# Performance work log

Hardware: AMD Instinct MI355X
Metric: run time of the kernel (lower is better)

## Reference

```python
import jax, jax.numpy as jnp
import numpy as np

NUM_HEADS = 16
SIGMA_DATA = 1.0


def setup_inputs() -> dict:
    key = jax.random.key(0)
    ks = jax.random.split(key, 6)
    B, N, C = 4, 2048, 1024
    x = jax.random.normal(ks[0], (B, N, C), dtype=jnp.float32)
    t = jax.random.uniform(ks[1], (B,), dtype=jnp.float32)
    # Linear layers stored as (in, out) so y = x @ W + b
    Wqkv = jax.random.normal(ks[2], (C, 3 * C), dtype=jnp.float32) * (C ** -0.5)
    bqkv = jax.random.normal(ks[3], (3 * C,), dtype=jnp.float32) * 0.02
    Wproj = jax.random.normal(ks[4], (C, C), dtype=jnp.float32) * (C ** -0.5)
    bproj = jax.random.normal(ks[5], (C,), dtype=jnp.float32) * 0.02
    return {"x": x, "t": t, "Wqkv": Wqkv, "bqkv": bqkv, "Wproj": Wproj, "bproj": bproj}


def reference(x, t, Wqkv, bqkv, Wproj, bproj):
    B, N, C = x.shape
    H = NUM_HEADS
    Dh = C // H
    scale = Dh ** -0.5

    qkv = (x @ Wqkv + bqkv).reshape(B, N, 3, H, Dh)
    qkv = jnp.transpose(qkv, (2, 0, 3, 1, 4))
    q, k, v = qkv[0], qkv[1], qkv[2]

    # softmax attention
    scores = jnp.einsum("bhmd,bhnd->bhmn", q, k) * scale
    attn = jax.nn.softmax(scores, axis=-1)
    o = jnp.einsum("bhmn,bhnd->bhmd", attn, v)          # [B, H, N, Dh]
    o = jnp.transpose(o, (0, 2, 1, 3)).reshape(B, N, C)  # [B, N, C]

    # rCM skip coefficients; kernel launch collapses per-batch coeffs to their mean (scalar)
    sd2 = SIGMA_DATA ** 2
    c_skip = (sd2 / (t * t + sd2)).mean()
    c_out = (SIGMA_DATA * t / jnp.sqrt(sd2 + t * t)).mean()

    out = c_skip * x + c_out * o  # fused epilogue
    return out @ Wproj + bproj
```

## Files before the change

### kernel.cpp

```cpp
#include <hip/hip_runtime.h>


typedef unsigned short ushort_t;
typedef __bf16 bf16x8 __attribute__((ext_vector_type(8)));
typedef float f32x4 __attribute__((ext_vector_type(4)));

#define GAS __attribute__((address_space(1)))
#define LAS __attribute__((address_space(3)))

static __device__ __forceinline__ ushort_t f2bf(float f) {
  union { float f; unsigned int u; } v; v.f = f;
  unsigned int r = v.u + 0x7fffu + ((v.u >> 16) & 1u);
  return (ushort_t)(r >> 16);
}

static __device__ __forceinline__ void async16(const void* g, void* l) {
  __builtin_amdgcn_global_load_lds((const GAS unsigned int*)g,
                                   (LAS unsigned int*)l, 16, 0, 0);
}

__global__ __launch_bounds__(256) void prep_kernel(
    const float* __restrict__ x, ushort_t* __restrict__ Xbf,
    const float* __restrict__ Wqkv, ushort_t* __restrict__ WqkvT,
    const float* __restrict__ Wproj, ushort_t* __restrict__ WprojT) {
  __shared__ float tile[32][33];
  const int bid = (int)blockIdx.x, tid = threadIdx.x;
  if (bid < 8192) {
    int i = (bid * 256 + tid) * 4;
    float4 v = *(const float4*)(x + i);
    ushort4 o = make_ushort4(f2bf(v.x), f2bf(v.y), f2bf(v.z), f2bf(v.w));
    *(ushort4*)(Xbf + i) = o;
    return;
  }
  const float* in;
  ushort_t* out;
  int R, C, bx, by;
  if (bid < 11264) {
    int q = bid - 8192;
    by = q / 96; bx = q - by * 96;
    in = Wqkv; out = WqkvT; R = 1024; C = 3072;
  } else {
    int p = bid - 11264;
    bx = p & 31; by = p >> 5;
    in = Wproj; out = WprojT; R = 1024; C = 1024;
  }
  int bc = bx * 32, br = by * 32;
  int tx = tid & 31, ty = tid >> 5;
#pragma unroll
  for (int i = 0; i < 32; i += 8)
    tile[ty + i][tx] = in[(size_t)(br + ty + i) * C + bc + tx];
  __syncthreads();
#pragma unroll
  for (int i = 0; i < 32; i += 8)
    out[(size_t)(bc + ty + i) * R + br + tx] = f2bf(tile[tx][ty + i]);
}

static __device__ __forceinline__ void gemm128_core(
    const ushort_t* __restrict__ A, const ushort_t* __restrict__ Bt, int K,
    int m0, int n0, ushort_t* As, ushort_t* Bs, f32x4 acc[4][4]) {
  const int tid = threadIdx.x;
  const int wave = tid >> 6, lane = tid & 63;
  const int wm = (wave >> 1) * 64, wn = (wave & 1) * 64;
  const int lr = lane & 15, quad = lane >> 4;
  const int ch = ((quad + (lr >> 1)) & 3) * 8;
  for (int kb = 0; kb < K; kb += 32) {
#pragma unroll
    for (int i = 0; i < 2; ++i) {
      int c = (i * 4 + wave) * 64 + lane;
      int row = c >> 2;
      int cg = (((c & 3) - ((c >> 3) & 3)) & 3) * 8;
      async16(A + (size_t)(m0 + row) * K + kb + cg, As + (i * 4 + wave) * 512);
      async16(Bt + (size_t)(n0 + row) * K + kb + cg, Bs + (i * 4 + wave) * 512);
    }
    __syncthreads();
    bf16x8 af[4], bfr[4];
#pragma unroll
    for (int i = 0; i < 4; ++i) {
      af[i]  = *(const bf16x8*)(As + (wm + i * 16 + lr) * 32 + ch);
      bfr[i] = *(const bf16x8*)(Bs + (wn + i * 16 + lr) * 32 + ch);
    }
#pragma unroll
    for (int i = 0; i < 4; ++i)
#pragma unroll
      for (int j = 0; j < 4; ++j)
        acc[i][j] = __builtin_amdgcn_mfma_f32_16x16x32_bf16(af[i], bfr[j], acc[i][j], 0, 0, 0);
    __syncthreads();
  }
}

__global__ __launch_bounds__(256) void gemm_qkv_kernel(
    const ushort_t* __restrict__ Xbf, const ushort_t* __restrict__ Wt,
    const float* __restrict__ bqkv, ushort_t* __restrict__ Qb,
    ushort_t* __restrict__ Kb, ushort_t* __restrict__ Vb) {
  __shared__ __align__(16) ushort_t As[128 * 32];
  __shared__ __align__(16) ushort_t Bs[128 * 32];
  const int m0 = (blockIdx.x & 63) << 7;
  const int n0 = (blockIdx.x >> 6) << 7;
  f32x4 acc[4][4];
#pragma unroll
  for (int i = 0; i < 4; ++i)
#pragma unroll
    for (int j = 0; j < 4; ++j) acc[i][j] = f32x4{0.f, 0.f, 0.f, 0.f};
  gemm128_core(Xbf, Wt, 1024, m0, n0, As, Bs, acc);

  const int tid = threadIdx.x, wave = tid >> 6, lane = tid & 63;
  const int wm = (wave >> 1) * 64, wn = (wave & 1) * 64;
  const int col = lane & 15, quad = lane >> 4;
  const int b = m0 >> 11;
  const float C1 = 0.18033688011112042f;
#pragma unroll
  for (int j = 0; j < 4; ++j) {
    int jc = n0 + wn + j * 16 + col;
    float bj = bqkv[jc];
    int which = jc >> 10, rem = jc & 1023;
    int hh = rem >> 6, d = rem & 63;
    if (which == 2) {
      size_t vb2 = ((size_t)(b * 16 + hh) * 64 + d) * 2048;
#pragma unroll
      for (int i = 0; i < 4; ++i) {
        int nbase = (m0 + wm + i * 16 + quad * 4) & 2047;
        int npos = (nbase & ~31) | (((nbase >> 2) & 3) << 3) | (((nbase >> 4) & 1) << 2);
        ushort4 pk = make_ushort4(f2bf(acc[i][j][0] + bj), f2bf(acc[i][j][1] + bj),
                                  f2bf(acc[i][j][2] + bj), f2bf(acc[i][j][3] + bj));
        *(ushort4*)(Vb + vb2 + npos) = pk;
      }
    } else {
      ushort_t* dst = which == 0 ? Qb : Kb;
      float sc = which == 0 ? C1 : 1.0f;
      size_t base = ((size_t)(b * 16 + hh) * 2048) * 64 + d;
#pragma unroll
      for (int i = 0; i < 4; ++i)
#pragma unroll
        for (int r = 0; r < 4; ++r) {
          int nseq = (m0 + wm + i * 16 + quad * 4 + r) & 2047;
          dst[base + (size_t)nseq * 64] = f2bf((acc[i][j][r] + bj) * sc);
        }
    }
  }
}

__global__ __launch_bounds__(256) void gemm_out_kernel(
    const ushort_t* __restrict__ Hbf, const ushort_t* __restrict__ Wt,
    const float* __restrict__ bproj, float* __restrict__ out) {
  __shared__ __align__(16) ushort_t As[128 * 32];
  __shared__ __align__(16) ushort_t Bs[128 * 32];
  const int m0 = (blockIdx.x & 63) << 7;
  const int n0 = (blockIdx.x >> 6) << 7;
  f32x4 acc[4][4];
#pragma unroll
  for (int i = 0; i < 4; ++i)
#pragma unroll
    for (int j = 0; j < 4; ++j) acc[i][j] = f32x4{0.f, 0.f, 0.f, 0.f};
  gemm128_core(Hbf, Wt, 1024, m0, n0, As, Bs, acc);

  const int tid = threadIdx.x, wave = tid >> 6, lane = tid & 63;
  const int wm = (wave >> 1) * 64, wn = (wave & 1) * 64;
  const int col = lane & 15, quad = lane >> 4;
#pragma unroll
  for (int j = 0; j < 4; ++j) {
    int jc = n0 + wn + j * 16 + col;
    float bj = bproj[jc];
#pragma unroll
    for (int i = 0; i < 4; ++i)
#pragma unroll
      for (int r = 0; r < 4; ++r) {
        int m = m0 + wm + i * 16 + quad * 4 + r;
        out[(size_t)m * 1024 + jc] = acc[i][j][r] + bj;
      }
  }
}

__global__ __launch_bounds__(256, 4) void attn_kernel(
    const ushort_t* __restrict__ Qb, const ushort_t* __restrict__ Kb,
    const ushort_t* __restrict__ Vb, const float* __restrict__ x,
    const float* __restrict__ t, ushort_t* __restrict__ Hbf) {
  __shared__ __align__(16) ushort_t Ks[2][64 * 64];
  __shared__ __align__(16) ushort_t Vs[2][64 * 64];

  const int tid = threadIdx.x, w = tid >> 6, lane = tid & 63;
  const int m = lane & 15, q = lane >> 4;
  const int bid = (int)blockIdx.x;
  const int wg = (bid & 7) * 128 + (bid >> 3);
  const int bh = wg >> 4, rowbase = ((wg & 15) << 7) + w * 32;

  const ushort_t* Qg = Qb + ((size_t)bh * 2048 + rowbase) * 64;
  const ushort_t* Kg = Kb + (size_t)bh * 2048 * 64;
  const ushort_t* Vg = Vb + (size_t)bh * 64 * 2048;

  bf16x8 qf[2][2];
#pragma unroll
  for (int qt = 0; qt < 2; ++qt) {
    qf[qt][0] = *(const bf16x8*)(Qg + (qt * 16 + m) * 64 + q * 8);
    qf[qt][1] = *(const bf16x8*)(Qg + (qt * 16 + m) * 64 + 32 + q * 8);
  }

  auto stage = [&](int kt, int buf) {
#pragma unroll
    for (int i = 0; i < 2; ++i) {
      int f = i * 256 + tid;
      int r = f >> 3, g = (f & 7) ^ (r & 7);
      async16(Kg + (size_t)(kt * 64 + r) * 64 + g * 8,
              Ks[buf] + (size_t)(i * 256 + w * 64) * 8);
    }
#pragma unroll
    for (int i = 0; i < 2; ++i) {
      int f = i * 256 + tid;
      int d = f >> 3, g = (f & 7) ^ (d & 7);
      async16(Vg + (size_t)d * 2048 + kt * 64 + g * 8,
              Vs[buf] + (size_t)(i * 256 + w * 64) * 8);
    }
  };
  stage(0, 0);

  f32x4 oacc[2][4], lacc[2];
#pragma unroll
  for (int qt = 0; qt < 2; ++qt) {
    lacc[qt] = f32x4{0.f, 0.f, 0.f, 0.f};
#pragma unroll
    for (int dt = 0; dt < 4; ++dt) oacc[qt][dt] = f32x4{0.f, 0.f, 0.f, 0.f};
  }

  const float C2 = -23.083120654223414f;
  const f32x4 c2v = {C2, C2, C2, C2};
  const int mk = m & 7;
  union { bf16x8 v; unsigned int u[4]; } onesu;
#pragma unroll
  for (int h = 0; h < 4; ++h) onesu.u[h] = 0x3F803F80u;
  const bf16x8 ones = onesu.v;

#pragma unroll 2
  for (int kt = 0; kt < 32; ++kt) {
    const int cur = kt & 1;
    __syncthreads();
    if (kt < 31) stage(kt + 1, cur ^ 1);
    const ushort_t* K0 = Ks[cur];
    const ushort_t* V0 = Vs[cur];

#pragma unroll
    for (int p = 0; p < 2; ++p) {
      f32x4 st[2][2];
#pragma unroll
      for (int sh = 0; sh < 2; ++sh) {
        int s = p * 2 + sh;
        bf16x8 kf0 = *(const bf16x8*)(K0 + (s * 16 + m) * 64 + (q ^ mk) * 8);
        bf16x8 kf1 = *(const bf16x8*)(K0 + (s * 16 + m) * 64 + ((q + 4) ^ mk) * 8);
#pragma unroll
        for (int qt = 0; qt < 2; ++qt) {
          f32x4 a = __builtin_amdgcn_mfma_f32_16x16x32_bf16(kf0, qf[qt][0], c2v, 0, 0, 0);
          st[sh][qt] = __builtin_amdgcn_mfma_f32_16x16x32_bf16(kf1, qf[qt][1], a, 0, 0, 0);
        }
      }
      bf16x8 pf[2];
#pragma unroll
      for (int qt = 0; qt < 2; ++qt) {
        float pv[8];
#pragma unroll
        for (int sh = 0; sh < 2; ++sh)
#pragma unroll
          for (int rr = 0; rr < 4; ++rr)
            pv[sh * 4 + rr] = __builtin_amdgcn_exp2f(st[sh][qt][rr]);
        union { bf16x8 v; unsigned int u[4]; } pk;
#pragma unroll
        for (int h = 0; h < 4; ++h)
          pk.u[h] = __builtin_amdgcn_perm(__float_as_uint(pv[2 * h + 1]),
                                          __float_as_uint(pv[2 * h]), 0x07060302);
        pf[qt] = pk.v;
      }
#pragma unroll
      for (int dt = 0; dt < 4; ++dt) {
        bf16x8 vf = *(const bf16x8*)(V0 + (dt * 16 + m) * 64 + ((p * 4 + q) ^ mk) * 8);
#pragma unroll
        for (int qt = 0; qt < 2; ++qt)
          oacc[qt][dt] = __builtin_amdgcn_mfma_f32_16x16x32_bf16(vf, pf[qt], oacc[qt][dt], 0, 0, 0);
      }
#pragma unroll
      for (int qt = 0; qt < 2; ++qt)
        lacc[qt] = __builtin_amdgcn_mfma_f32_16x16x32_bf16(ones, pf[qt], lacc[qt], 0, 0, 0);
    }
  }

  float cs = 0.f, co = 0.f;
#pragma unroll
  for (int i = 0; i < 4; ++i) {
    float ti = t[i];
    float d = 1.f + ti * ti;
    cs += 1.f / d;
    co += ti / sqrtf(d);
  }
  cs *= 0.25f; co *= 0.25f;

  const int b = bh >> 4, hh = bh & 15;
#pragma unroll
  for (int qt = 0; qt < 2; ++qt) {
    float inv = co / lacc[qt][0];
    int nseq = rowbase + qt * 16 + m;
#pragma unroll
    for (int dt = 0; dt < 4; ++dt) {
      int c0 = hh * 64 + dt * 16 + q * 4;
      size_t midx = ((size_t)b * 2048 + nseq) * 1024 + c0;
      float4 xv = *(const float4*)(x + midx);
      ushort4 hv = make_ushort4(f2bf(cs * xv.x + oacc[qt][dt][0] * inv),
                                f2bf(cs * xv.y + oacc[qt][dt][1] * inv),
                                f2bf(cs * xv.z + oacc[qt][dt][2] * inv),
                                f2bf(cs * xv.w + oacc[qt][dt][3] * inv));
      *(ushort4*)(Hbf + midx) = hv;
    }
  }
}

extern "C" void kernel_launch(void* const* d_in, const int* in_sizes, int n_in,
                              void* d_out, int out_size, void* d_ws, size_t ws_size,
                              hipStream_t stream) {
  const float* x     = (const float*)d_in[0];
  const float* t     = (const float*)d_in[1];
  const float* Wqkv  = (const float*)d_in[2];
  const float* bqkv  = (const float*)d_in[3];
  const float* Wproj = (const float*)d_in[4];
  const float* bproj = (const float*)d_in[5];
  float* out = (float*)d_out;
  char* ws = (char*)d_ws;

  ushort_t* Xbf    = (ushort_t*)(ws + 256);
  ushort_t* WqkvT  = (ushort_t*)(ws + 256 + 16777216);
  ushort_t* WprojT = (ushort_t*)(ws + 256 + 16777216 + 6291456);
  ushort_t* Qb     = (ushort_t*)(ws + 256 + 16777216 + 6291456 + 2097152);
  ushort_t* Kb = Qb + 8388608;
  ushort_t* Vb = Kb + 8388608;
  ushort_t* Hb = Vb + 8388608;

  prep_kernel<<<12288, 256, 0, stream>>>(x, Xbf, Wqkv, WqkvT, Wproj, WprojT);
  gemm_qkv_kernel<<<1536, 256, 0, stream>>>(Xbf, WqkvT, bqkv, Qb, Kb, Vb);
  attn_kernel<<<1024, 256, 0, stream>>>(Qb, Kb, Vb, x, t, Hb);
  gemm_out_kernel<<<512, 256, 0, stream>>>(Hb, WprojT, bproj, out);
}
```

Measured before the change: 265.4 us.

## Use 256x128 double-buffered GEMM tiles with K=64 and XOR-swizzled LDS

Both projection GEMMs move from 128x128 blocks with 256 threads to 256x128 blocks with 512 threads and a K-step of 64. The LDS tiles are double-buffered, so the next tile's async global-to-LDS load is issued while the current one is consumed, with one barrier per step. An XOR swizzle is applied to LDS chunks to avoid bank conflicts. The larger tiles need much more shared memory, which lowers occupancy, and the output GEMM grid shrinks to 256 blocks.

```diff
diff --git a/kernel.cpp b/kernel.cpp
--- a/kernel.cpp
+++ b/kernel.cpp
@@ -55,62 +55,92 @@
     out[(size_t)(bc + ty + i) * R + br + tx] = f2bf(tile[tx][ty + i]);
 }
 
-static __device__ __forceinline__ void gemm128_core(
+static __device__ __forceinline__ void gemm256_core(
     const ushort_t* __restrict__ A, const ushort_t* __restrict__ Bt, int K,
     int m0, int n0, ushort_t* As, ushort_t* Bs, f32x4 acc[4][4]) {
   const int tid = threadIdx.x;
   const int wave = tid >> 6, lane = tid & 63;
-  const int wm = (wave >> 1) * 64, wn = (wave & 1) * 64;
+  const int wm = (wave >> 1) * 64;
+  const int wn = (wave & 1) * 64;
   const int lr = lane & 15, quad = lane >> 4;
-  const int ch = ((quad + (lr >> 1)) & 3) * 8;
-  for (int kb = 0; kb < K; kb += 32) {
-#pragma unroll
-    for (int i = 0; i < 2; ++i) {
-      int c = (i * 4 + wave) * 64 + lane;
-      int row = c >> 2;
-      int cg = (((c & 3) - ((c >> 3) & 3)) & 3) * 8;
-      async16(A + (size_t)(m0 + row) * K + kb + cg, As + (i * 4 + wave) * 512);
-      async16(Bt + (size_t)(n0 + row) * K + kb + cg, Bs + (i * 4 + wave) * 512);
-    }
+  const int lmask = lr & 7;
+
+  const int f0 = tid;
+  auto stageA = [&](int kb, int buf, int u) {
+    int f = u * 512 + f0;
+    int r = f >> 3, g = (f & 7) ^ (r & 7);
+    async16(A + (size_t)(m0 + r) * K + kb + g * 8,
+            As + buf * (256 * 64) + (u * 512 + wave * 64) * 8);
+  };
+  auto stageB = [&](int kb, int buf, int u) {
+    int f = u * 512 + f0;
+    int r = f >> 3, g = (f & 7) ^ (r & 7);
+    async16(Bt + (size_t)(n0 + r) * K + kb + g * 8,
+            Bs + buf * (128 * 64) + (u * 512 + wave * 64) * 8);
+  };
+  auto stage_tile = [&](int kb, int buf) {
+#pragma unroll
+    for (int u = 0; u < 4; ++u) stageA(kb, buf, u);
+#pragma unroll
+    for (int u = 0; u < 2; ++u) stageB(kb, buf, u);
+  };
+
+  stage_tile(0, 0);
+  const int nt = K >> 6;
+  for (int t = 0; t < nt; ++t) {
+    const int cur = t & 1;
     __syncthreads();
-    bf16x8 af[4], bfr[4];
-#pragma unroll
-    for (int i = 0; i < 4; ++i) {
-      af[i]  = *(const bf16x8*)(As + (wm + i * 16 + lr) * 32 + ch);
-      bfr[i] = *(const bf16x8*)(Bs + (wn + i * 16 + lr) * 32 + ch);
-    }
+    if (t + 1 < nt) stage_tile((t + 1) << 6, cur ^ 1);
+    const ushort_t* As0 = As + cur * (256 * 64);
+    const ushort_t* Bs0 = Bs + cur * (128 * 64);
+    bf16x8 af[4][2], bf[4][2];
 #pragma unroll
     for (int i = 0; i < 4; ++i)
 #pragma unroll
+      for (int ks = 0; ks < 2; ++ks)
+        af[i][ks] = *(const bf16x8*)(As0 + (wm + i * 16 + lr) * 64 +
+                                     (((ks * 4 + quad) ^ lmask) * 8));
+#pragma unroll
+    for (int j = 0; j < 4; ++j)
+#pragma unroll
+      for (int ks = 0; ks < 2; ++ks)
+        bf[j][ks] = *(const bf16x8*)(Bs0 + (wn + j * 16 + lr) * 64 +
+                                     (((ks * 4 + quad) ^ lmask) * 8));
+#pragma unroll
+    for (int i = 0; i < 4; ++i)
+#pragma unroll
       for (int j = 0; j < 4; ++j)
-        acc[i][j] = __builtin_amdgcn_mfma_f32_16x16x32_bf16(af[i], bfr[j], acc[i][j], 0, 0, 0);
-    __syncthreads();
-  }
-}
-
-__global__ __launch_bounds__(256) void gemm_qkv_kernel(
+#pragma unroll
+        for (int ks = 0; ks < 2; ++ks)
+          acc[i][j] = __builtin_amdgcn_mfma_f32_16x16x32_bf16(af[i][ks], bf[j][ks],
+                                                              acc[i][j], 0, 0, 0);
+  }
+}
+
+__global__ __launch_bounds__(512, 2) void gemm_qkv_kernel(
     const ushort_t* __restrict__ Xbf, const ushort_t* __restrict__ Wt,
     const float* __restrict__ bqkv, ushort_t* __restrict__ Qb,
     ushort_t* __restrict__ Kb, ushort_t* __restrict__ Vb) {
-  __shared__ __align__(16) ushort_t As[128 * 32];
-  __shared__ __align__(16) ushort_t Bs[128 * 32];
-  const int m0 = (blockIdx.x & 63) << 7;
-  const int n0 = (blockIdx.x >> 6) << 7;
+  __shared__ __align__(16) ushort_t As[2 * 256 * 64];
+  __shared__ __align__(16) ushort_t Bs[2 * 128 * 64];
+  const int bid = (int)blockIdx.x;
+  const int m0 = (bid & 31) << 8;
+  const int n0 = (bid >> 5) << 7;
   f32x4 acc[4][4];
 #pragma unroll
   for (int i = 0; i < 4; ++i)
 #pragma unroll
     for (int j = 0; j < 4; ++j) acc[i][j] = f32x4{0.f, 0.f, 0.f, 0.f};
-  gemm128_core(Xbf, Wt, 1024, m0, n0, As, Bs, acc);
+  gemm256_core(Xbf, Wt, 1024, m0, n0, As, Bs, acc);
 
   const int tid = threadIdx.x, wave = tid >> 6, lane = tid & 63;
-  const int wm = (wave >> 1) * 64, wn = (wave & 1) * 64;
+  const int wme = (wave >> 1) * 64, wne = (wave & 1) * 64;
   const int col = lane & 15, quad = lane >> 4;
   const int b = m0 >> 11;
   const float C1 = 0.18033688011112042f;
 #pragma unroll
   for (int j = 0; j < 4; ++j) {
-    int jc = n0 + wn + j * 16 + col;
+    int jc = n0 + wne + j * 16 + col;
     float bj = bqkv[jc];
     int which = jc >> 10, rem = jc & 1023;
     int hh = rem >> 6, d = rem & 63;
@@ -118,7 +148,7 @@
       size_t vb2 = ((size_t)(b * 16 + hh) * 64 + d) * 2048;
 #pragma unroll
       for (int i = 0; i < 4; ++i) {
-        int nbase = (m0 + wm + i * 16 + quad * 4) & 2047;
+        int nbase = (m0 + wme + i * 16 + quad * 4) & 2047;
         int npos = (nbase & ~31) | (((nbase >> 2) & 3) << 3) | (((nbase >> 4) & 1) << 2);
         ushort4 pk = make_ushort4(f2bf(acc[i][j][0] + bj), f2bf(acc[i][j][1] + bj),
                                   f2bf(acc[i][j][2] + bj), f2bf(acc[i][j][3] + bj));
@@ -132,39 +162,40 @@
       for (int i = 0; i < 4; ++i)
 #pragma unroll
         for (int r = 0; r < 4; ++r) {
-          int nseq = (m0 + wm + i * 16 + quad * 4 + r) & 2047;
+          int nseq = (m0 + wme + i * 16 + quad * 4 + r) & 2047;
           dst[base + (size_t)nseq * 64] = f2bf((acc[i][j][r] + bj) * sc);
         }
     }
   }
 }
 
-__global__ __launch_bounds__(256) void gemm_out_kernel(
+__global__ __launch_bounds__(512, 2) void gemm_out_kernel(
     const ushort_t* __restrict__ Hbf, const ushort_t* __restrict__ Wt,
     const float* __restrict__ bproj, float* __restrict__ out) {
-  __shared__ __align__(16) ushort_t As[128 * 32];
-  __shared__ __align__(16) ushort_t Bs[128 * 32];
-  const int m0 = (blockIdx.x & 63) << 7;
-  const int n0 = (blockIdx.x >> 6) << 7;
+  __shared__ __align__(16) ushort_t As[2 * 256 * 64];
+  __shared__ __align__(16) ushort_t Bs[2 * 128 * 64];
+  const int bid = (int)blockIdx.x;
+  const int m0 = (bid & 31) << 8;
+  const int n0 = (bid >> 5) << 7;
   f32x4 acc[4][4];
 #pragma unroll
   for (int i = 0; i < 4; ++i)
 #pragma unroll
     for (int j = 0; j < 4; ++j) acc[i][j] = f32x4{0.f, 0.f, 0.f, 0.f};
-  gemm128_core(Hbf, Wt, 1024, m0, n0, As, Bs, acc);
+  gemm256_core(Hbf, Wt, 1024, m0, n0, As, Bs, acc);
 
   const int tid = threadIdx.x, wave = tid >> 6, lane = tid & 63;
-  const int wm = (wave >> 1) * 64, wn = (wave & 1) * 64;
+  const int wme = (wave >> 1) * 64, wne = (wave & 1) * 64;
   const int col = lane & 15, quad = lane >> 4;
 #pragma unroll
   for (int j = 0; j < 4; ++j) {
-    int jc = n0 + wn + j * 16 + col;
+    int jc = n0 + wne + j * 16 + col;
     float bj = bproj[jc];
 #pragma unroll
     for (int i = 0; i < 4; ++i)
 #pragma unroll
       for (int r = 0; r < 4; ++r) {
-        int m = m0 + wm + i * 16 + quad * 4 + r;
+        int m = m0 + wme + i * 16 + quad * 4 + r;
         out[(size_t)m * 1024 + jc] = acc[i][j][r] + bj;
       }
   }
@@ -329,7 +360,7 @@
   ushort_t* Hb = Vb + 8388608;
 
   prep_kernel<<<12288, 256, 0, stream>>>(x, Xbf, Wqkv, WqkvT, Wproj, WprojT);
-  gemm_qkv_kernel<<<1536, 256, 0, stream>>>(Xbf, WqkvT, bqkv, Qb, Kb, Vb);
+  gemm_qkv_kernel<<<768, 512, 0, stream>>>(Xbf, WqkvT, bqkv, Qb, Kb, Vb);
   attn_kernel<<<1024, 256, 0, stream>>>(Qb, Kb, Vb, x, t, Hb);
-  gemm_out_kernel<<<512, 256, 0, stream>>>(Hb, WprojT, bproj, out);
-}
+  gemm_out_kernel<<<256, 512, 0, stream>>>(Hb, WprojT, bproj, out);
+}
```

New measurement: 279.3 us. +5.3%, slower.

## Rewrite GEMMs as single-wave 64x64 tiles with double-buffered async LDS loads

Applied to the files above, without the earlier changes.

Both the QKV and output-projection GEMMs move from 256-thread blocks computing 128x128 tiles to 64-thread single-wave blocks computing 64x64 tiles, launched on four times as many blocks. The K loop now double-buffers LDS and drops __syncthreads, using s_waitcnt vmcnt to overlap the next tile's global-to-LDS load with the MFMAs. The aim is to hide load latency and remove barrier cost. The trade-off is that each 64x64 tile reuses loaded data less than a 128x128 tile, so global and L2 traffic roughly doubles. The pipeline also relies on each wave seeing only its own LDS writes, which holds because each block is one wave.

```diff
diff --git a/kernel.cpp b/kernel.cpp
--- a/kernel.cpp
+++ b/kernel.cpp
@@ -55,62 +55,71 @@
     out[(size_t)(bc + ty + i) * R + br + tx] = f2bf(tile[tx][ty + i]);
 }
 
-static __device__ __forceinline__ void gemm128_core(
+static __device__ __forceinline__ void gemm64_core(
     const ushort_t* __restrict__ A, const ushort_t* __restrict__ Bt, int K,
     int m0, int n0, ushort_t* As, ushort_t* Bs, f32x4 acc[4][4]) {
-  const int tid = threadIdx.x;
-  const int wave = tid >> 6, lane = tid & 63;
-  const int wm = (wave >> 1) * 64, wn = (wave & 1) * 64;
+  const int lane = threadIdx.x & 63;
   const int lr = lane & 15, quad = lane >> 4;
-  const int ch = ((quad + (lr >> 1)) & 3) * 8;
-  for (int kb = 0; kb < K; kb += 32) {
-#pragma unroll
-    for (int i = 0; i < 2; ++i) {
-      int c = (i * 4 + wave) * 64 + lane;
-      int row = c >> 2;
-      int cg = (((c & 3) - ((c >> 3) & 3)) & 3) * 8;
-      async16(A + (size_t)(m0 + row) * K + kb + cg, As + (i * 4 + wave) * 512);
-      async16(Bt + (size_t)(n0 + row) * K + kb + cg, Bs + (i * 4 + wave) * 512);
-    }
-    __syncthreads();
+
+  auto stage = [&](int kb, int buf) {
+#pragma unroll
+    for (int u = 0; u < 4; ++u) {
+      int f = u * 64 + lane;
+      int r = f >> 2;
+      int cg = (((f & 3) - (r & 3)) & 3) * 8;
+      async16(A + (size_t)(m0 + r) * K + kb + cg, As + buf * 2048 + u * 512);
+      async16(Bt + (size_t)(n0 + r) * K + kb + cg, Bs + buf * 2048 + u * 512);
+    }
+  };
+  stage(0, 0);
+  stage(32, 1);
+
+  const int nk = K >> 5;
+  for (int t = 0; t < nk; ++t) {
+    if (t + 1 < nk) asm volatile("s_waitcnt vmcnt(8)" ::: "memory");
+    else            asm volatile("s_waitcnt vmcnt(0)" ::: "memory");
+    const ushort_t* As0 = As + (t & 1) * 2048;
+    const ushort_t* Bs0 = Bs + (t & 1) * 2048;
     bf16x8 af[4], bfr[4];
 #pragma unroll
     for (int i = 0; i < 4; ++i) {
-      af[i]  = *(const bf16x8*)(As + (wm + i * 16 + lr) * 32 + ch);
-      bfr[i] = *(const bf16x8*)(Bs + (wn + i * 16 + lr) * 32 + ch);
+      int row = i * 16 + lr;
+      int ch = ((quad + row) & 3) * 8;
+      af[i]  = *(const bf16x8*)(As0 + row * 32 + ch);
+      bfr[i] = *(const bf16x8*)(Bs0 + row * 32 + ch);
     }
 #pragma unroll
     for (int i = 0; i < 4; ++i)
 #pragma unroll
       for (int j = 0; j < 4; ++j)
         acc[i][j] = __builtin_amdgcn_mfma_f32_16x16x32_bf16(af[i], bfr[j], acc[i][j], 0, 0, 0);
-    __syncthreads();
-  }
-}
-
-__global__ __launch_bounds__(256) void gemm_qkv_kernel(
+    if (t + 2 < nk) stage((t + 2) << 5, t & 1);
+  }
+}
+
+__global__ __launch_bounds__(64, 4) void gemm_qkv_kernel(
     const ushort_t* __restrict__ Xbf, const ushort_t* __restrict__ Wt,
     const float* __restrict__ bqkv, ushort_t* __restrict__ Qb,
     ushort_t* __restrict__ Kb, ushort_t* __restrict__ Vb) {
-  __shared__ __align__(16) ushort_t As[128 * 32];
-  __shared__ __align__(16) ushort_t Bs[128 * 32];
-  const int m0 = (blockIdx.x & 63) << 7;
-  const int n0 = (blockIdx.x >> 6) << 7;
+  __shared__ __align__(16) ushort_t As[2 * 64 * 32];
+  __shared__ __align__(16) ushort_t Bs[2 * 64 * 32];
+  const int bid = (int)blockIdx.x;
+  const int m0 = (bid & 127) << 6;
+  const int n0 = (bid >> 7) << 6;
   f32x4 acc[4][4];
 #pragma unroll
   for (int i = 0; i < 4; ++i)
 #pragma unroll
     for (int j = 0; j < 4; ++j) acc[i][j] = f32x4{0.f, 0.f, 0.f, 0.f};
-  gemm128_core(Xbf, Wt, 1024, m0, n0, As, Bs, acc);
-
-  const int tid = threadIdx.x, wave = tid >> 6, lane = tid & 63;
-  const int wm = (wave >> 1) * 64, wn = (wave & 1) * 64;
+  gemm64_core(Xbf, Wt, 1024, m0, n0, As, Bs, acc);
+
+  const int lane = threadIdx.x & 63;
   const int col = lane & 15, quad = lane >> 4;
   const int b = m0 >> 11;
   const float C1 = 0.18033688011112042f;
 #pragma unroll
   for (int j = 0; j < 4; ++j) {
-    int jc = n0 + wn + j * 16 + col;
+    int jc = n0 + j * 16 + col;
     float bj = bqkv[jc];
     int which = jc >> 10, rem = jc & 1023;
     int hh = rem >> 6, d = rem & 63;
@@ -118,7 +127,7 @@
       size_t vb2 = ((size_t)(b * 16 + hh) * 64 + d) * 2048;
 #pragma unroll
       for (int i = 0; i < 4; ++i) {
-        int nbase = (m0 + wm + i * 16 + quad * 4) & 2047;
+        int nbase = (m0 + i * 16 + quad * 4) & 2047;
         int npos = (nbase & ~31) | (((nbase >> 2) & 3) << 3) | (((nbase >> 4) & 1) << 2);
         ushort4 pk = make_ushort4(f2bf(acc[i][j][0] + bj), f2bf(acc[i][j][1] + bj),
                                   f2bf(acc[i][j][2] + bj), f2bf(acc[i][j][3] + bj));
@@ -132,39 +141,39 @@
       for (int i = 0; i < 4; ++i)
 #pragma unroll
         for (int r = 0; r < 4; ++r) {
-          int nseq = (m0 + wm + i * 16 + quad * 4 + r) & 2047;
+          int nseq = (m0 + i * 16 + quad * 4 + r) & 2047;
           dst[base + (size_t)nseq * 64] = f2bf((acc[i][j][r] + bj) * sc);
         }
     }
   }
 }
 
-__global__ __launch_bounds__(256) void gemm_out_kernel(
+__global__ __launch_bounds__(64, 4) void gemm_out_kernel(
     const ushort_t* __restrict__ Hbf, const ushort_t* __restrict__ Wt,
     const float* __restrict__ bproj, float* __restrict__ out) {
-  __shared__ __align__(16) ushort_t As[128 * 32];
-  __shared__ __align__(16) ushort_t Bs[128 * 32];
-  const int m0 = (blockIdx.x & 63) << 7;
-  const int n0 = (blockIdx.x >> 6) << 7;
+  __shared__ __align__(16) ushort_t As[2 * 64 * 32];
+  __shared__ __align__(16) ushort_t Bs[2 * 64 * 32];
+  const int bid = (int)blockIdx.x;
+  const int m0 = (bid & 127) << 6;
+  const int n0 = (bid >> 7) << 6;
   f32x4 acc[4][4];
 #pragma unroll
   for (int i = 0; i < 4; ++i)
 #pragma unroll
     for (int j = 0; j < 4; ++j) acc[i][j] = f32x4{0.f, 0.f, 0.f, 0.f};
-  gemm128_core(Hbf, Wt, 1024, m0, n0, As, Bs, acc);
-
-  const int tid = threadIdx.x, wave = tid >> 6, lane = tid & 63;
-  const int wm = (wave >> 1) * 64, wn = (wave & 1) * 64;
+  gemm64_core(Hbf, Wt, 1024, m0, n0, As, Bs, acc);
+
+  const int lane = threadIdx.x & 63;
   const int col = lane & 15, quad = lane >> 4;
 #pragma unroll
   for (int j = 0; j < 4; ++j) {
-    int jc = n0 + wn + j * 16 + col;
+    int jc = n0 + j * 16 + col;
     float bj = bproj[jc];
 #pragma unroll
     for (int i = 0; i < 4; ++i)
 #pragma unroll
       for (int r = 0; r < 4; ++r) {
-        int m = m0 + wm + i * 16 + quad * 4 + r;
+        int m = m0 + i * 16 + quad * 4 + r;
         out[(size_t)m * 1024 + jc] = acc[i][j][r] + bj;
       }
   }
@@ -329,7 +338,7 @@
   ushort_t* Hb = Vb + 8388608;
 
   prep_kernel<<<12288, 256, 0, stream>>>(x, Xbf, Wqkv, WqkvT, Wproj, WprojT);
-  gemm_qkv_kernel<<<1536, 256, 0, stream>>>(Xbf, WqkvT, bqkv, Qb, Kb, Vb);
+  gemm_qkv_kernel<<<6144, 64, 0, stream>>>(Xbf, WqkvT, bqkv, Qb, Kb, Vb);
   attn_kernel<<<1024, 256, 0, stream>>>(Qb, Kb, Vb, x, t, Hb);
-  gemm_out_kernel<<<512, 256, 0, stream>>>(Hb, WprojT, bproj, out);
-}
+  gemm_out_kernel<<<2048, 64, 0, stream>>>(Hb, WprojT, bproj, out);
+}
```

New measurement: 302.1 us. +13.8%, slower.
